# Kernel tuning notes

Hardware: AMD Instinct MI355X
Metric: run time of the kernel (lower is better)

Reference implementation:

```python
import jax, jax.numpy as jnp
import numpy as np

N, D, N_CLASSES = 4096, 256, 64
MARGIN = 0.2


def setup_inputs() -> dict:
    key = jax.random.key(0)
    k1, k2 = jax.random.split(key)
    embeddings = jax.random.normal(k1, (N, D), dtype=jnp.float32)
    labels = jax.random.randint(k2, (N,), 0, N_CLASSES)
    same = labels[:, None] == labels[None, :]
    eye = jnp.eye(N, dtype=bool)
    return {
        "embeddings": embeddings,
        "positives_mask": same & ~eye,
        "negatives_mask": ~same,
    }


def reference(embeddings, positives_mask, negatives_mask):
    # Pairwise squared L2 distances (LpDistance, normalize_embeddings=False)
    sq = jnp.sum(embeddings * embeddings, axis=1)  # [N]
    d2 = sq[:, None] + sq[None, :] - 2.0 * (embeddings @ embeddings.T)  # [N,N]
    d2 = jnp.maximum(d2, 0.0)

    # Batch-hard mining (argmax/argmin on squared dists == on L2 dists)
    hp = jnp.argmax(jnp.where(positives_mask, d2, -jnp.inf), axis=1)  # hardest positive per anchor
    hn = jnp.argmin(jnp.where(negatives_mask, d2, jnp.inf), axis=1)   # hardest negative per anchor
    rows = jnp.arange(N)

    d_ap = jnp.sqrt(d2[rows, hp])
    d_an = jnp.sqrt(d2[rows, hn])
    d_pn = jnp.sqrt(d2[hp, hn])

    # TripletMarginLoss with swap=True: use min(d(a,n), d(p,n))
    d_an_eff = jnp.minimum(d_an, d_pn)
    l = jax.nn.relu(d_ap - d_an_eff + MARGIN)  # [N] per-anchor triplet loss

    # Only anchors with >=1 positive and >=1 negative form valid triplets
    valid = jnp.any(positives_mask, axis=1) & jnp.any(negatives_mask, axis=1)
    nonzero = (l > 0) & valid
    cnt = jnp.sum(nonzero).astype(jnp.float32)
    total = jnp.sum(jnp.where(nonzero, l, 0.0))
    # AvgNonZeroReducer: mean over strictly-positive losses; 0 if none
    return jnp.where(cnt > 0, total / jnp.maximum(cnt, 1.0), 0.0)
```

## Files before the change

kernel.cpp:

```cpp
#include <hip/hip_runtime.h>
#include <math.h>


#define NN 4096
#define DD 256
#define MARGIN 0.2f
#define NCHUNK 32
#define BK 64

typedef _Float16 f16;
typedef __attribute__((ext_vector_type(8))) _Float16 f16x8;
typedef __attribute__((ext_vector_type(4))) _Float16 f16x4;
typedef __attribute__((ext_vector_type(4))) float f32x4;
typedef unsigned long long u64;
typedef unsigned int u32;

#define OFF_SQ     64
#define OFF_EH     (OFF_SQ + NN * 4)
#define OFF_POSB   (OFF_EH + NN * DD * 2)
#define OFF_PPK    (OFF_POSB + (NN * (long)NN / 8))
#define OFF_PNK    (OFF_PPK + NN * NCHUNK * 8)
#define OFF_LOSS   (OFF_PNK + NN * NCHUNK * 8)

#define CONV_BLOCKS   (NN / 4)
#define REPACK_BLOCKS 4096
#define PREP_BLOCKS   (CONV_BLOCKS + REPACK_BLOCKS)
#define RP_WAVES      (REPACK_BLOCKS * 4)

__device__ __forceinline__ int swz(int r) { return (r ^ (r >> 3)) & 7; }

__device__ __forceinline__ void dma16(const void* g, void* l) {
  __builtin_amdgcn_global_load_lds(
      (const __attribute__((address_space(1))) void*)g,
      (__attribute__((address_space(3))) void*)l, 16, 0, 0);
}

__global__ __launch_bounds__(256)
void prep_kernel(const float* __restrict__ E, const void* __restrict__ pos_raw,
                 f16* __restrict__ Eh, float* __restrict__ sq,
                 u64* __restrict__ posb) {
  const int bid = blockIdx.x;
  const int tid = threadIdx.x;
  if (bid < CONV_BLOCKS) {
    const int row = bid * 4 + (tid >> 6);
    const int lane = tid & 63;
    const float4 v = *(const float4*)&E[(size_t)row * DD + lane * 4];
    f16x4 h;
    h[0] = (f16)v.x; h[1] = (f16)v.y; h[2] = (f16)v.z; h[3] = (f16)v.w;
    *(f16x4*)&Eh[(size_t)row * DD + lane * 4] = h;
    float s = v.x * v.x + v.y * v.y + v.z * v.z + v.w * v.w;
#pragma unroll
    for (int off = 32; off > 0; off >>= 1) s += __shfl_down(s, off);
    if (lane == 0) sq[row] = s;
    return;
  }

  __shared__ int s_ev[4];
  int ev = 0;
#pragma unroll
  for (int k = 0; k < 16; ++k) {
    const int di = tid + (k << 8);
    const u32 v = ((const u32*)pos_raw)[di];
    if (v & 0xffffff00u) ev |= 1;
    if (v == 0x3f800000u) ev |= 2;
    if (di & 1) {
      if (v == 0x3ff00000u) ev |= 4;
      if (v) ev |= 8;
    }
  }
#pragma unroll
  for (int off = 32; off > 0; off >>= 1) ev |= __shfl_xor(ev, off);
  if ((tid & 63) == 0) s_ev[tid >> 6] = ev;
  __syncthreads();
  ev = s_ev[0] | s_ev[1] | s_ev[2] | s_ev[3];
  int f;
  if (ev & 2) f = 2;
  else if (ev & 4) f = 4;
  else if (ev & 1) f = 1;
  else if (ev & 8) f = 0;
  else f = 3;

  const int lane = tid & 63;
  const int wid = (bid - CONV_BLOCKS) * 4 + (tid >> 6);

  if (f == 0 || f == 2) {
    const int nspan = NN * NN / 256;
    for (int s = wid; s < nspan; s += RP_WAVES) {
      const size_t eb = (size_t)s * 256 + lane * 4;
      u32 p;
      if (f == 0) {
        const uint4 v = *(const uint4*)((const u32*)pos_raw + eb);
        p = (v.x != 0u) | ((v.y != 0u) << 1) | ((v.z != 0u) << 2) | ((v.w != 0u) << 3);
      } else {
        const float4 v = *(const float4*)((const float*)pos_raw + eb);
        p = (v.x != 0.f) | ((v.y != 0.f) << 1) | ((v.z != 0.f) << 2) | ((v.w != 0.f) << 3);
      }
      u64 val = (u64)p << (4 * (lane & 15));
#pragma unroll
      for (int off = 1; off < 16; off <<= 1) val |= __shfl_xor(val, off);
      if ((lane & 15) == 0) posb[(size_t)s * 4 + (lane >> 4)] = val;
    }
  } else if (f == 1) {
    const int nspan = NN * NN / 1024;
    for (int s = wid; s < nspan; s += RP_WAVES) {
      const size_t eb = (size_t)s * 1024 + lane * 16;
      const uint4 v = *(const uint4*)((const unsigned char*)pos_raw + eb);
      u32 bits = 0;
      const u32 d[4] = {v.x, v.y, v.z, v.w};
#pragma unroll
      for (int c = 0; c < 4; ++c)
#pragma unroll
        for (int b = 0; b < 4; ++b)
          bits |= (u32)(((d[c] >> (8 * b)) & 0xffu) != 0u) << (c * 4 + b);
      u64 val = (u64)bits << (16 * (lane & 3));
#pragma unroll
      for (int off = 1; off < 4; off <<= 1) val |= __shfl_xor(val, off);
      if ((lane & 3) == 0) posb[(size_t)s * 16 + (lane >> 2)] = val;
    }
  } else {
    const long long stride = (long long)REPACK_BLOCKS * 256;
    const long long base = (long long)(bid - CONV_BLOCKS) * 256 + tid;
#pragma unroll
    for (int it = 0; it < 16; ++it) {
      const long long idx = base + it * stride;
      bool p;
      if (f == 3) p = ((const u64*)pos_raw)[idx] != 0ull;
      else        p = ((const double*)pos_raw)[idx] != 0.0;
      const u64 w = __ballot(p);
      if ((tid & 63) == 0) posb[idx >> 6] = w;
    }
  }
}

__global__ __launch_bounds__(256)
void mine_kernel(const f16* __restrict__ Eh, const float* __restrict__ sq,
                 const u64* __restrict__ posb,
                 u64* __restrict__ part_p, u64* __restrict__ part_n) {
  __shared__ union {
    struct { f16 A[128 * BK]; f16 B[128 * BK]; } t;
    struct { u64 pk[2][128]; u64 nk[2][128]; } r;
  } sm;

  const int tid = threadIdx.x;
  const int lane = tid & 63, wave = tid >> 6;
  const int lx = lane & 15, q = lane >> 4;
  const int wr = wave >> 1, wc = wave & 1;
  const int ib = blockIdx.x & 31, jb = blockIdx.x >> 5;
  const int i0 = ib * 128, j0 = jb * 128;

  f32x4 acc[4][4];
#pragma unroll
  for (int mt = 0; mt < 4; ++mt)
#pragma unroll
    for (int nt = 0; nt < 4; ++nt) acc[mt][nt] = (f32x4)0.f;

  const int drow = lane >> 3;
  const int dslot = lane & 7;

  for (int kk = 0; kk < DD; kk += BK) {
    __syncthreads();
#pragma unroll
    for (int t = 0; t < 4; ++t) {
      const int i = wave * 4 + t;
      const int r = i * 8 + drow;
      const int g = dslot ^ swz(r);
      dma16(Eh + (size_t)(i0 + r) * DD + kk + g * 8, &sm.t.A[i * 512]);
      dma16(Eh + (size_t)(j0 + r) * DD + kk + g * 8, &sm.t.B[i * 512]);
    }
    __syncthreads();
#pragma unroll
    for (int ss = 0; ss < 2; ++ss) {
      f16x8 af[4], bf[4];
#pragma unroll
      for (int mt = 0; mt < 4; ++mt) {
        const int r = wr * 64 + mt * 16 + lx;
        af[mt] = *(const f16x8*)&sm.t.A[r * BK + (((ss * 4 + q) ^ swz(r)) << 3)];
      }
#pragma unroll
      for (int nt = 0; nt < 4; ++nt) {
        const int r = wc * 64 + nt * 16 + lx;
        bf[nt] = *(const f16x8*)&sm.t.B[r * BK + (((ss * 4 + q) ^ swz(r)) << 3)];
      }
#pragma unroll
      for (int mt = 0; mt < 4; ++mt)
#pragma unroll
        for (int nt = 0; nt < 4; ++nt)
          acc[mt][nt] = __builtin_amdgcn_mfma_f32_16x16x32_f16(bf[nt], af[mt], acc[mt][nt], 0, 0, 0);
    }
  }

  float sqi_[4];
  u64 pw_[4], nw_[4];
  const int jw = (j0 + wc * 64) >> 6;
#pragma unroll
  for (int mt = 0; mt < 4; ++mt) {
    const int gi = i0 + wr * 64 + mt * 16 + lx;
    sqi_[mt] = sq[gi];
    const u64 pw = posb[(size_t)gi * (NN / 64) + jw];
    const u64 eye = ((gi >> 6) == jw) ? (1ull << (gi & 63)) : 0ull;
    pw_[mt] = pw;
    nw_[mt] = ~(pw | eye);
  }
  f32x4 sqjv[4];
#pragma unroll
  for (int nt = 0; nt < 4; ++nt)
    sqjv[nt] = *(const f32x4*)&sq[j0 + wc * 64 + nt * 16 + q * 4];
  const u32 jlo_base = ~(u32)(j0 + wc * 64 + q * 4);

  u64 pk[4] = {0ull, 0ull, 0ull, 0ull};
  u64 nk[4] = {0ull, 0ull, 0ull, 0ull};
#pragma unroll
  for (int mt = 0; mt < 4; ++mt) {
#pragma unroll
    for (int nt = 0; nt < 4; ++nt) {
#pragma unroll
      for (int r = 0; r < 4; ++r) {
        const int c = nt * 16 + q * 4 + r;
        const float d2 = fmaxf(fmaf(-2.f, acc[mt][nt][r], sqi_[mt] + sqjv[nt][r]), 0.f);
        const u32 hi = __float_as_uint(d2);
        const u32 lo = jlo_base - (u32)(nt * 16 + r);
        const u64 key = ((u64)hi << 32) | lo;
        const u64 nkey = ((u64)(~hi) << 32) | lo;
        if ((pw_[mt] >> c) & 1ull) pk[mt] = key > pk[mt] ? key : pk[mt];
        if ((nw_[mt] >> c) & 1ull) nk[mt] = nkey > nk[mt] ? nkey : nk[mt];
      }
    }
  }
#pragma unroll
  for (int mt = 0; mt < 4; ++mt) {
#pragma unroll
    for (int off = 16; off < 64; off <<= 1) {
      u64 o = __shfl_xor(pk[mt], off);
      if (o > pk[mt]) pk[mt] = o;
      o = __shfl_xor(nk[mt], off);
      if (o > nk[mt]) nk[mt] = o;
    }
  }

  __syncthreads();
  if (q == 0) {
#pragma unroll
    for (int mt = 0; mt < 4; ++mt) {
      const int lr = wr * 64 + mt * 16 + lx;
      sm.r.pk[wc][lr] = pk[mt];
      sm.r.nk[wc][lr] = nk[mt];
    }
  }
  __syncthreads();
  if (tid < 128) {
    const u64 p0 = sm.r.pk[0][tid], p1 = sm.r.pk[1][tid];
    const u64 n0 = sm.r.nk[0][tid], n1 = sm.r.nk[1][tid];
    part_p[(size_t)jb * NN + i0 + tid] = p0 > p1 ? p0 : p1;
    part_n[(size_t)jb * NN + i0 + tid] = n0 > n1 ? n0 : n1;
  }
}

__global__ __launch_bounds__(256)
void finalize_kernel(const float* __restrict__ E, const float* __restrict__ sq,
                     const u64* __restrict__ part_p, const u64* __restrict__ part_n,
                     float* __restrict__ loss) {
  const int tid = threadIdx.x;
  const int a = blockIdx.x * 4 + (tid >> 6);
  const int lane = tid & 63;
  const int ch = lane & 31;
  u64 key = (lane < 32) ? part_p[(size_t)ch * NN + a] : part_n[(size_t)ch * NN + a];
#pragma unroll
  for (int off = 1; off < 32; off <<= 1) {
    const u64 o = __shfl_xor(key, off);
    if (o > key) key = o;
  }
  const u64 pkey = __shfl(key, 0);
  const u64 nkey = __shfl(key, 32);
  const bool valid = (pkey != 0ull) && (nkey != 0ull);
  const int p = (int)(~(u32)pkey);
  const int n = (int)(~(u32)nkey);
  const int pp = valid ? p : 0, nn = valid ? n : 0;

  const float4 xa = *(const float4*)&E[(size_t)a * DD + lane * 4];
  const float4 xp = *(const float4*)&E[(size_t)pp * DD + lane * 4];
  const float4 xn = *(const float4*)&E[(size_t)nn * DD + lane * 4];
  float dap = xa.x * xp.x + xa.y * xp.y + xa.z * xp.z + xa.w * xp.w;
  float dan = xa.x * xn.x + xa.y * xn.y + xa.z * xn.z + xa.w * xn.w;
  float dpn = xp.x * xn.x + xp.y * xn.y + xp.z * xn.z + xp.w * xn.w;
#pragma unroll
  for (int off = 32; off > 0; off >>= 1) {
    dap += __shfl_down(dap, off);
    dan += __shfl_down(dan, off);
    dpn += __shfl_down(dpn, off);
  }
  if (lane == 0) {
    float l = 0.f;
    if (valid) {
      const float d2ap = fmaxf(sq[a] + sq[pp] - 2.f * dap, 0.f);
      const float d2an = fmaxf(sq[a] + sq[nn] - 2.f * dan, 0.f);
      const float d2pn = fmaxf(sq[pp] + sq[nn] - 2.f * dpn, 0.f);
      l = fmaxf(sqrtf(d2ap) - fminf(sqrtf(d2an), sqrtf(d2pn)) + MARGIN, 0.f);
    }
    loss[a] = l;
  }
}

__global__ __launch_bounds__(1024)
void reduce_kernel(const float* __restrict__ loss, float* __restrict__ out) {
  __shared__ float s_sum[16], s_cnt[16];
  const int tid = threadIdx.x;
  const float4 v = *(const float4*)&loss[tid * 4];
  float s = v.x + v.y + v.z + v.w;
  float c = (v.x > 0.f) + (v.y > 0.f) + (v.z > 0.f) + (v.w > 0.f);
#pragma unroll
  for (int off = 32; off > 0; off >>= 1) {
    s += __shfl_down(s, off);
    c += __shfl_down(c, off);
  }
  if ((tid & 63) == 0) { s_sum[tid >> 6] = s; s_cnt[tid >> 6] = c; }
  __syncthreads();
  if (tid == 0) {
    float ts = 0.f, tc = 0.f;
#pragma unroll
    for (int w = 0; w < 16; ++w) { ts += s_sum[w]; tc += s_cnt[w]; }
    out[0] = (tc > 0.f) ? (ts / fmaxf(tc, 1.f)) : 0.f;
  }
}

extern "C" void kernel_launch(void* const* d_in, const int* in_sizes, int n_in,
                              void* d_out, int out_size, void* d_ws, size_t ws_size,
                              hipStream_t stream) {
  const float* E = (const float*)d_in[0];
  const void* posm = d_in[1];
  float* out = (float*)d_out;
  char* ws = (char*)d_ws;

  float* sq = (float*)(ws + OFF_SQ);
  f16* Eh = (f16*)(ws + OFF_EH);
  u64* posb = (u64*)(ws + OFF_POSB);
  u64* ppk = (u64*)(ws + OFF_PPK);
  u64* pnk = (u64*)(ws + OFF_PNK);
  float* loss = (float*)(ws + OFF_LOSS);

  prep_kernel<<<PREP_BLOCKS, 256, 0, stream>>>(E, posm, Eh, sq, posb);
  mine_kernel<<<32 * NCHUNK, 256, 0, stream>>>(Eh, sq, posb, ppk, pnk);
  finalize_kernel<<<NN / 4, 256, 0, stream>>>(E, sq, ppk, pnk, loss);
  reduce_kernel<<<1, 1024, 0, stream>>>(loss, out);
}
```

Measured before the change: 166.8 us.

## Shrink mining tiles to 64x64 with full-K single-shot LDS load

The mining kernel now uses 64x64 output tiles instead of 128x128, which gives 4096 blocks instead of 1024. Each block loads the entire 256-wide K dimension into LDS in one pass with a new XOR swizzle, replacing the looped 64-wide K chunks and their per-chunk barriers. The finalize kernel now reduces 64 partial chunks per anchor, handling positive and negative keys at the same time. The goals are better occupancy and latency hiding and fewer synchronisations. The costs are less operand reuse per block and twice the partial-result traffic.

```diff
diff --git a/kernel.cpp b/kernel.cpp
--- a/kernel.cpp
+++ b/kernel.cpp
@@ -5,8 +5,7 @@
 #define NN 4096
 #define DD 256
 #define MARGIN 0.2f
-#define NCHUNK 32
-#define BK 64
+#define NCHUNK 64
 
 typedef _Float16 f16;
 typedef __attribute__((ext_vector_type(8))) _Float16 f16x8;
@@ -26,8 +25,6 @@
 #define REPACK_BLOCKS 4096
 #define PREP_BLOCKS   (CONV_BLOCKS + REPACK_BLOCKS)
 #define RP_WAVES      (REPACK_BLOCKS * 4)
-
-__device__ __forceinline__ int swz(int r) { return (r ^ (r >> 3)) & 7; }
 
 __device__ __forceinline__ void dma16(const void* g, void* l) {
   __builtin_amdgcn_global_load_lds(
@@ -137,85 +134,82 @@
                  const u64* __restrict__ posb,
                  u64* __restrict__ part_p, u64* __restrict__ part_n) {
   __shared__ union {
-    struct { f16 A[128 * BK]; f16 B[128 * BK]; } t;
-    struct { u64 pk[2][128]; u64 nk[2][128]; } r;
+    struct { f16 A[64 * 256]; f16 B[64 * 256]; } t;
+    struct { u64 pk[2][64]; u64 nk[2][64]; } r;
   } sm;
 
   const int tid = threadIdx.x;
   const int lane = tid & 63, wave = tid >> 6;
   const int lx = lane & 15, q = lane >> 4;
   const int wr = wave >> 1, wc = wave & 1;
-  const int ib = blockIdx.x & 31, jb = blockIdx.x >> 5;
-  const int i0 = ib * 128, j0 = jb * 128;
-
-  f32x4 acc[4][4];
-#pragma unroll
-  for (int mt = 0; mt < 4; ++mt)
-#pragma unroll
-    for (int nt = 0; nt < 4; ++nt) acc[mt][nt] = (f32x4)0.f;
-
-  const int drow = lane >> 3;
-  const int dslot = lane & 7;
-
-  for (int kk = 0; kk < DD; kk += BK) {
-    __syncthreads();
-#pragma unroll
-    for (int t = 0; t < 4; ++t) {
-      const int i = wave * 4 + t;
-      const int r = i * 8 + drow;
-      const int g = dslot ^ swz(r);
-      dma16(Eh + (size_t)(i0 + r) * DD + kk + g * 8, &sm.t.A[i * 512]);
-      dma16(Eh + (size_t)(j0 + r) * DD + kk + g * 8, &sm.t.B[i * 512]);
-    }
-    __syncthreads();
-#pragma unroll
-    for (int ss = 0; ss < 2; ++ss) {
-      f16x8 af[4], bf[4];
-#pragma unroll
-      for (int mt = 0; mt < 4; ++mt) {
-        const int r = wr * 64 + mt * 16 + lx;
-        af[mt] = *(const f16x8*)&sm.t.A[r * BK + (((ss * 4 + q) ^ swz(r)) << 3)];
-      }
-#pragma unroll
-      for (int nt = 0; nt < 4; ++nt) {
-        const int r = wc * 64 + nt * 16 + lx;
-        bf[nt] = *(const f16x8*)&sm.t.B[r * BK + (((ss * 4 + q) ^ swz(r)) << 3)];
-      }
-#pragma unroll
-      for (int mt = 0; mt < 4; ++mt)
-#pragma unroll
-        for (int nt = 0; nt < 4; ++nt)
-          acc[mt][nt] = __builtin_amdgcn_mfma_f32_16x16x32_f16(bf[nt], af[mt], acc[mt][nt], 0, 0, 0);
-    }
-  }
-
-  float sqi_[4];
-  u64 pw_[4], nw_[4];
-  const int jw = (j0 + wc * 64) >> 6;
-#pragma unroll
-  for (int mt = 0; mt < 4; ++mt) {
-    const int gi = i0 + wr * 64 + mt * 16 + lx;
+  const int ib = blockIdx.x & 63, jb = blockIdx.x >> 6;
+  const int i0 = ib * 64, j0 = jb * 64;
+
+  const int drow = lane >> 5;
+  const int dslot = lane & 31;
+#pragma unroll
+  for (int t = 0; t < 8; ++t) {
+    const int i2 = wave * 8 + t;
+    const int r = i2 * 2 + drow;
+    const int g = dslot ^ (r & 31);
+    dma16(Eh + (size_t)(i0 + r) * DD + g * 8, &sm.t.A[i2 * 512]);
+    dma16(Eh + (size_t)(j0 + r) * DD + g * 8, &sm.t.B[i2 * 512]);
+  }
+  __syncthreads();
+
+  f32x4 acc[2][2];
+#pragma unroll
+  for (int mt = 0; mt < 2; ++mt)
+#pragma unroll
+    for (int nt = 0; nt < 2; ++nt) acc[mt][nt] = (f32x4)0.f;
+
+#pragma unroll
+  for (int ks = 0; ks < 8; ++ks) {
+    f16x8 af[2], bf[2];
+#pragma unroll
+    for (int mt = 0; mt < 2; ++mt) {
+      const int r = wr * 32 + mt * 16 + lx;
+      af[mt] = *(const f16x8*)&sm.t.A[r * 256 + (((ks * 4 + q) ^ (r & 31)) << 3)];
+    }
+#pragma unroll
+    for (int nt = 0; nt < 2; ++nt) {
+      const int r = wc * 32 + nt * 16 + lx;
+      bf[nt] = *(const f16x8*)&sm.t.B[r * 256 + (((ks * 4 + q) ^ (r & 31)) << 3)];
+    }
+#pragma unroll
+    for (int mt = 0; mt < 2; ++mt)
+#pragma unroll
+      for (int nt = 0; nt < 2; ++nt)
+        acc[mt][nt] = __builtin_amdgcn_mfma_f32_16x16x32_f16(bf[nt], af[mt], acc[mt][nt], 0, 0, 0);
+  }
+
+  float sqi_[2];
+  u64 pw_[2], nw_[2];
+  const int jw = j0 >> 6;
+#pragma unroll
+  for (int mt = 0; mt < 2; ++mt) {
+    const int gi = i0 + wr * 32 + mt * 16 + lx;
     sqi_[mt] = sq[gi];
     const u64 pw = posb[(size_t)gi * (NN / 64) + jw];
     const u64 eye = ((gi >> 6) == jw) ? (1ull << (gi & 63)) : 0ull;
     pw_[mt] = pw;
     nw_[mt] = ~(pw | eye);
   }
-  f32x4 sqjv[4];
-#pragma unroll
-  for (int nt = 0; nt < 4; ++nt)
-    sqjv[nt] = *(const f32x4*)&sq[j0 + wc * 64 + nt * 16 + q * 4];
-  const u32 jlo_base = ~(u32)(j0 + wc * 64 + q * 4);
-
-  u64 pk[4] = {0ull, 0ull, 0ull, 0ull};
-  u64 nk[4] = {0ull, 0ull, 0ull, 0ull};
-#pragma unroll
-  for (int mt = 0; mt < 4; ++mt) {
-#pragma unroll
-    for (int nt = 0; nt < 4; ++nt) {
+  f32x4 sqjv[2];
+#pragma unroll
+  for (int nt = 0; nt < 2; ++nt)
+    sqjv[nt] = *(const f32x4*)&sq[j0 + wc * 32 + nt * 16 + q * 4];
+  const u32 jlo_base = ~(u32)(j0 + wc * 32 + q * 4);
+
+  u64 pk[2] = {0ull, 0ull};
+  u64 nk[2] = {0ull, 0ull};
+#pragma unroll
+  for (int mt = 0; mt < 2; ++mt) {
+#pragma unroll
+    for (int nt = 0; nt < 2; ++nt) {
 #pragma unroll
       for (int r = 0; r < 4; ++r) {
-        const int c = nt * 16 + q * 4 + r;
+        const int c = wc * 32 + nt * 16 + q * 4 + r;
         const float d2 = fmaxf(fmaf(-2.f, acc[mt][nt][r], sqi_[mt] + sqjv[nt][r]), 0.f);
         const u32 hi = __float_as_uint(d2);
         const u32 lo = jlo_base - (u32)(nt * 16 + r);
@@ -227,7 +221,7 @@
     }
   }
 #pragma unroll
-  for (int mt = 0; mt < 4; ++mt) {
+  for (int mt = 0; mt < 2; ++mt) {
 #pragma unroll
     for (int off = 16; off < 64; off <<= 1) {
       u64 o = __shfl_xor(pk[mt], off);
@@ -240,14 +234,14 @@
   __syncthreads();
   if (q == 0) {
 #pragma unroll
-    for (int mt = 0; mt < 4; ++mt) {
-      const int lr = wr * 64 + mt * 16 + lx;
+    for (int mt = 0; mt < 2; ++mt) {
+      const int lr = wr * 32 + mt * 16 + lx;
       sm.r.pk[wc][lr] = pk[mt];
       sm.r.nk[wc][lr] = nk[mt];
     }
   }
   __syncthreads();
-  if (tid < 128) {
+  if (tid < 64) {
     const u64 p0 = sm.r.pk[0][tid], p1 = sm.r.pk[1][tid];
     const u64 n0 = sm.r.nk[0][tid], n1 = sm.r.nk[1][tid];
     part_p[(size_t)jb * NN + i0 + tid] = p0 > p1 ? p0 : p1;
@@ -262,15 +256,15 @@
   const int tid = threadIdx.x;
   const int a = blockIdx.x * 4 + (tid >> 6);
   const int lane = tid & 63;
-  const int ch = lane & 31;
-  u64 key = (lane < 32) ? part_p[(size_t)ch * NN + a] : part_n[(size_t)ch * NN + a];
-#pragma unroll
-  for (int off = 1; off < 32; off <<= 1) {
-    const u64 o = __shfl_xor(key, off);
-    if (o > key) key = o;
-  }
-  const u64 pkey = __shfl(key, 0);
-  const u64 nkey = __shfl(key, 32);
+  u64 pkey = part_p[(size_t)lane * NN + a];
+  u64 nkey = part_n[(size_t)lane * NN + a];
+#pragma unroll
+  for (int off = 1; off < 64; off <<= 1) {
+    const u64 po = __shfl_xor(pkey, off);
+    if (po > pkey) pkey = po;
+    const u64 no = __shfl_xor(nkey, off);
+    if (no > nkey) nkey = no;
+  }
   const bool valid = (pkey != 0ull) && (nkey != 0ull);
   const int p = (int)(~(u32)pkey);
   const int n = (int)(~(u32)nkey);
@@ -338,7 +332,7 @@
   float* loss = (float*)(ws + OFF_LOSS);
 
   prep_kernel<<<PREP_BLOCKS, 256, 0, stream>>>(E, posm, Eh, sq, posb);
-  mine_kernel<<<32 * NCHUNK, 256, 0, stream>>>(Eh, sq, posb, ppk, pnk);
+  mine_kernel<<<64 * NCHUNK, 256, 0, stream>>>(Eh, sq, posb, ppk, pnk);
   finalize_kernel<<<NN / 4, 256, 0, stream>>>(E, sq, ppk, pnk, loss);
   reduce_kernel<<<1, 1024, 0, stream>>>(loss, out);
 }
```

Result: slower. 181.8 us (+9.0%).
